# Performance work log

Hardware: AMD Instinct MI355X
Metric: run time of the kernel (lower is better)

The kernel has to match this reference:

```python
import jax, jax.numpy as jnp
import numpy as np

B, T, C, H, S = 4, 2048, 1024, 16, 64
LN_EPS = 1e-5
WKV_EPS = 1e-6
K_CLAMP = 30.0


def _ln(x, g, b):
    m = jnp.mean(x, axis=-1, keepdims=True)
    v = jnp.var(x, axis=-1, keepdims=True)
    return (x - m) * jax.lax.rsqrt(v + LN_EPS) * g + b


def _wkv(k, v, time_decay, time_first):
    # k, v: [B,T,H,S]; recurrence in fp32 over time
    decay = jnp.exp(-jnp.exp(time_decay.astype(jnp.float32)))  # [H,S]
    tf = jnp.exp(time_first.astype(jnp.float32))               # [H,S]
    kt = jnp.moveaxis(k, 1, 0).astype(jnp.float32)  # [T,B,H,S]
    vt = jnp.moveaxis(v, 1, 0).astype(jnp.float32)
    # t == 0 special case: state seeded with time_first factor
    w0 = jnp.exp(jnp.minimum(kt[0], K_CLAMP))
    num0 = tf * w0 * vt[0]
    den0 = tf * w0

    def step(carry, xs):
        num, den = carry
        kk, vv = xs
        w = jnp.exp(jnp.minimum(kk, K_CLAMP))
        num = decay * num + w * vv
        den = decay * den + w
        return (num, den), num / (den + WKV_EPS)

    (_, _), rest = jax.lax.scan(step, (num0, den0), (kt[1:], vt[1:]))
    out = jnp.concatenate([(num0 / (den0 + WKV_EPS))[None], rest], axis=0)  # [T,B,H,S]
    return jnp.moveaxis(out, 0, 1)  # [B,T,H,S]


def setup_inputs() -> dict:
    key = jax.random.key(0)
    ks = jax.random.split(key, 8)
    sc = 1.0 / np.sqrt(C)
    sc4 = 1.0 / np.sqrt(4 * C)
    return {
        "x": jax.random.normal(ks[0], (B, T, C), jnp.float32),
        "time_decay": jnp.full((H, S), -5.0, jnp.float32),
        "time_first": jnp.zeros((H, S), jnp.float32),
        "Wk": jax.random.normal(ks[1], (C, C), jnp.float32) * sc,
        "Wv": jax.random.normal(ks[2], (C, C), jnp.float32) * sc,
        "Wr": jax.random.normal(ks[3], (C, C), jnp.float32) * sc,
        "Wo": jax.random.normal(ks[4], (C, C), jnp.float32) * sc,
        "Wffk": jax.random.normal(ks[5], (4 * C, C), jnp.float32) * sc,
        "Wffv": jax.random.normal(ks[6], (C, 4 * C), jnp.float32) * sc4,
        "ln1_g": jnp.ones((C,), jnp.float32),
        "ln1_b": jnp.zeros((C,), jnp.float32),
        "ln2_g": jnp.ones((C,), jnp.float32),
        "ln2_b": jnp.zeros((C,), jnp.float32),
    }


def reference(x, time_decay, time_first, Wk, Wv, Wr, Wo, Wffk, Wffv, ln1_g, ln1_b, ln2_g, ln2_b):
    b, t, c = x.shape
    h, s = time_decay.shape
    xl = _ln(x, ln1_g, ln1_b)
    k = (xl @ Wk.T).reshape(b, t, h, s)
    v = (xl @ Wv.T).reshape(b, t, h, s)
    r = (xl @ Wr.T).reshape(b, t, h, s)
    wkv = _wkv(k, v, time_decay, time_first).astype(x.dtype)
    rwkv = (jax.nn.sigmoid(r) * wkv).reshape(b, t, c)
    x = x + rwkv @ Wo.T
    xl2 = _ln(x, ln2_g, ln2_b)
    ffn = (jax.nn.relu(xl2 @ Wffk.T) ** 2) @ Wffv.T
    return x + ffn
```

## Files before the change

### kernel.cpp

```cpp
#include <hip/hip_runtime.h>
#include <cstdint>
#include <cstddef>

#define TT 2048
#define CC 1024
#define HH 16
#define SS 64
#define MROWS 8192
#define KVRN 3072
#define NCH 32
#define LCH 64

using short8 = __attribute__((ext_vector_type(8))) short;
using f32x4  = __attribute__((ext_vector_type(4))) float;

__device__ __forceinline__ float b2f(unsigned short u) {
  union { unsigned int i; float f; } c; c.i = ((unsigned int)u) << 16; return c.f;
}
__device__ __forceinline__ unsigned short f2b(float f) {
  union { float f; unsigned int i; } c; c.f = f;
  unsigned int r = c.i + 0x7fffu + ((c.i >> 16) & 1u);
  return (unsigned short)(r >> 16);
}

typedef const __attribute__((address_space(1))) unsigned int* gas_ptr;
typedef __attribute__((address_space(3))) unsigned int* las_ptr;
__device__ __forceinline__ void gl_lds16(const unsigned short* g, unsigned short* l) {
  __builtin_amdgcn_global_load_lds((gas_ptr)g, (las_ptr)l, 16, 0, 0);
}

__global__ __launch_bounds__(256) void cvt_ln_kernel(const float* __restrict__ Wk,
                                                     const float* __restrict__ Wv,
                                                     const float* __restrict__ Wr,
                                                     const float* __restrict__ Wo,
                                                     const float* __restrict__ Wffk,
                                                     const float* __restrict__ Wffv,
                                                     unsigned short* __restrict__ dst,
                                                     const float* __restrict__ x,
                                                     const float* __restrict__ g,
                                                     const float* __restrict__ bta,
                                                     unsigned short* __restrict__ xlo,
                                                     float* __restrict__ x2o) {
  const size_t M1 = 1048576;
  const int tid = threadIdx.x;
  if (blockIdx.x < 12288) {
    size_t i = ((size_t)blockIdx.x * 256 + tid) * 4;
    const float* src; size_t off;
    if      (i <  1 * M1) { src = Wk;   off = 0;      }
    else if (i <  2 * M1) { src = Wv;   off = 1 * M1; }
    else if (i <  3 * M1) { src = Wr;   off = 2 * M1; }
    else if (i <  4 * M1) { src = Wo;   off = 3 * M1; }
    else if (i <  8 * M1) { src = Wffk; off = 4 * M1; }
    else                  { src = Wffv; off = 8 * M1; }
    float4 v = *(const float4*)(src + (i - off));
    *(ushort4*)(dst + i) = make_ushort4(f2b(v.x), f2b(v.y), f2b(v.z), f2b(v.w));
    return;
  }
  const int row = blockIdx.x - 12288;
  const float* xr = x + (size_t)row * CC;
  float4 v = *(const float4*)(xr + tid * 4);
  *(float4*)(x2o + (size_t)row * CC + tid * 4) = v;
  float s  = v.x + v.y + v.z + v.w;
  float ss = v.x * v.x + v.y * v.y + v.z * v.z + v.w * v.w;
#pragma unroll
  for (int off = 32; off > 0; off >>= 1) {
    s  += __shfl_xor(s, off, 64);
    ss += __shfl_xor(ss, off, 64);
  }
  __shared__ float ls[4], lss[4];
  if ((tid & 63) == 0) { ls[tid >> 6] = s; lss[tid >> 6] = ss; }
  __syncthreads();
  s  = ls[0] + ls[1] + ls[2] + ls[3];
  ss = lss[0] + lss[1] + lss[2] + lss[3];
  const float mean = s * (1.0f / CC);
  const float var  = ss * (1.0f / CC) - mean * mean;
  const float rstd = rsqrtf(var + 1e-5f);
  float4 gv = *(const float4*)(g + tid * 4);
  float4 bv = *(const float4*)(bta + tid * 4);
  ushort4 o = make_ushort4(f2b((v.x - mean) * rstd * gv.x + bv.x),
                           f2b((v.y - mean) * rstd * gv.y + bv.y),
                           f2b((v.z - mean) * rstd * gv.z + bv.z),
                           f2b((v.w - mean) * rstd * gv.w + bv.w));
  *(ushort4*)(xlo + (size_t)row * CC + tid * 4) = o;
}

__global__ __launch_bounds__(256) void ln_kernel(const float* __restrict__ x,
                                                 const float* __restrict__ g,
                                                 const float* __restrict__ bta,
                                                 unsigned short* __restrict__ out,
                                                 float* __restrict__ outc) {
  const int row = blockIdx.x;
  const int tid = threadIdx.x;
  const float* xr = x + (size_t)row * CC;
  float4 v = *(const float4*)(xr + tid * 4);
  *(float4*)(outc + (size_t)row * CC + tid * 4) = v;
  float s  = v.x + v.y + v.z + v.w;
  float ss = v.x * v.x + v.y * v.y + v.z * v.z + v.w * v.w;
#pragma unroll
  for (int off = 32; off > 0; off >>= 1) {
    s  += __shfl_xor(s, off, 64);
    ss += __shfl_xor(ss, off, 64);
  }
  __shared__ float ls[4], lss[4];
  if ((tid & 63) == 0) { ls[tid >> 6] = s; lss[tid >> 6] = ss; }
  __syncthreads();
  s  = ls[0] + ls[1] + ls[2] + ls[3];
  ss = lss[0] + lss[1] + lss[2] + lss[3];
  const float mean = s * (1.0f / CC);
  const float var  = ss * (1.0f / CC) - mean * mean;
  const float rstd = rsqrtf(var + 1e-5f);
  float4 gv = *(const float4*)(g + tid * 4);
  float4 bv = *(const float4*)(bta + tid * 4);
  ushort4 o = make_ushort4(f2b((v.x - mean) * rstd * gv.x + bv.x),
                           f2b((v.y - mean) * rstd * gv.y + bv.y),
                           f2b((v.z - mean) * rstd * gv.z + bv.z),
                           f2b((v.w - mean) * rstd * gv.w + bv.w));
  *(ushort4*)(out + (size_t)row * CC + tid * 4) = o;
}

__global__ __launch_bounds__(64) void wkv_local(const unsigned short* __restrict__ kvr,
                                                const float* __restrict__ td,
                                                const float* __restrict__ tfp,
                                                float* __restrict__ scratch) {
  const int blk = blockIdx.x;
  const int bh = blk >> 5, c = blk & (NCH - 1);
  const int b = bh >> 4, h = bh & 15;
  const int s = threadIdx.x;
  const int ch = h * SS + s;
  const float e = __expf(td[ch]);
  const float d = __expf(-e);
  const float tfir = __expf(tfp[ch]);
  size_t idx = ((size_t)b * TT + (size_t)c * LCH) * KVRN + ch;
  float num = 0.f, den = 0.f;
  for (int i = 0; i < LCH; ++i) {
    float w = __expf(fminf(b2f(kvr[idx]), 30.f));
    if (c == 0 && i == 0) w *= tfir;
    float vv = b2f(kvr[idx + 1024]);
    num = d * num + w * vv;
    den = d * den + w;
    idx += KVRN;
  }
  float* o = scratch + ((size_t)bh * NCH + c) * 128;
  o[s] = num; o[64 + s] = den;
}

__global__ __launch_bounds__(64) void wkv_emit(const unsigned short* __restrict__ kvr,
                                               const float* __restrict__ td,
                                               const float* __restrict__ tfp,
                                               const float* __restrict__ scratch,
                                               unsigned short* __restrict__ rwkv) {
  const int blk = blockIdx.x;
  const int bh = blk >> 5, c = blk & (NCH - 1);
  const int b = bh >> 4, h = bh & 15;
  const int s = threadIdx.x;
  const int ch = h * SS + s;
  const float e = __expf(td[ch]);
  const float d = __expf(-e);
  const float Dc = __expf(-e * (float)LCH);
  const float tfir = __expf(tfp[ch]);
  float num = 0.f, den = 0.f;
  const float* sc = scratch + (size_t)bh * NCH * 128;
  for (int cc = 0; cc < c; ++cc) {
    num = Dc * num + sc[cc * 128 + s];
    den = Dc * den + sc[cc * 128 + 64 + s];
  }
  size_t idx = ((size_t)b * TT + (size_t)c * LCH) * KVRN + ch;
  size_t odx = ((size_t)b * TT + (size_t)c * LCH) * CC + ch;
  for (int i = 0; i < LCH; ++i) {
    float w = __expf(fminf(b2f(kvr[idx]), 30.f));
    if (c == 0 && i == 0) w *= tfir;
    float vv = b2f(kvr[idx + 1024]);
    num = d * num + w * vv;
    den = d * den + w;
    float o = num / (den + 1e-6f);
    float rr = b2f(kvr[idx + 2048]);
    float sg = 1.0f / (1.0f + __expf(-rr));
    rwkv[odx] = f2b(sg * o);
    idx += KVRN;
    odx += CC;
  }
}

template <int EP>
__global__ __launch_bounds__(256, 3) void gemm_bt(const unsigned short* __restrict__ A,
                                                  const unsigned short* __restrict__ Bw,
                                                  void* __restrict__ outv,
                                                  const float* __restrict__ res,
                                                  int N, int K) {
  __shared__ __align__(16) unsigned short As[3][128 * 32];
  __shared__ __align__(16) unsigned short Bs[3][128 * 32];
  const int tid = threadIdx.x;

  const int nbn = N >> 7;
  const int per_grp = nbn << 4;
  const int bid = blockIdx.x;
  const int grp = bid / per_grp;
  const int rem = bid - grp * per_grp;
  const int bm = (grp << 4) + (rem & 15);
  const int bn = rem >> 4;

  const int ch0 = tid, ch1 = tid + 256;
  const int r0 = ch0 >> 2, q0 = (ch0 & 3) ^ ((ch0 >> 3) & 3);
  const int r1 = ch1 >> 2, q1 = (ch1 & 3) ^ ((ch1 >> 3) & 3);
  const unsigned short* ga0 = A  + (size_t)(bm * 128 + r0) * K + q0 * 8;
  const unsigned short* ga1 = A  + (size_t)(bm * 128 + r1) * K + q1 * 8;
  const unsigned short* gb0 = Bw + (size_t)(bn * 128 + r0) * K + q0 * 8;
  const unsigned short* gb1 = Bw + (size_t)(bn * 128 + r1) * K + q1 * 8;
  const int so0 = ch0 * 8, so1 = ch1 * 8;

  const int lane = tid & 63;
  const int w    = tid >> 6;
  const int q    = lane >> 4, r16 = lane & 15;
  const int qs   = q ^ ((r16 >> 1) & 3);
  const int wrow = (w >> 1) * 64, wcol = (w & 1) * 64;

  f32x4 acc[4][4] = {};

  auto stage = [&](int b3) {
    gl_lds16(ga0, &As[b3][so0]);
    gl_lds16(ga1, &As[b3][so1]);
    gl_lds16(gb0, &Bs[b3][so0]);
    gl_lds16(gb1, &Bs[b3][so1]);
    ga0 += 32; ga1 += 32; gb0 += 32; gb1 += 32;
  };

  const int iters = K >> 5;
  stage(0);
  stage(1);

  int cb = 0, pb = 2;
  for (int i = 0; i < iters; ++i) {
    __builtin_amdgcn_s_waitcnt(0x0F74);
    __builtin_amdgcn_sched_barrier(0);
    asm volatile("s_barrier");
    __builtin_amdgcn_sched_barrier(0);
    if (i + 2 < iters) stage(pb);

    const unsigned short* Ab = &As[cb][0];
    const unsigned short* Bb = &Bs[cb][0];
    short8 af[4], bfr[4];
#pragma unroll
    for (int mi = 0; mi < 4; ++mi)
      af[mi] = *(const short8*)(Ab + ((wrow + mi * 16 + r16) * 4 + qs) * 8);
#pragma unroll
    for (int ni = 0; ni < 4; ++ni)
      bfr[ni] = *(const short8*)(Bb + ((wcol + ni * 16 + r16) * 4 + qs) * 8);
#pragma unroll
    for (int mi = 0; mi < 4; ++mi)
#pragma unroll
      for (int ni = 0; ni < 4; ++ni)
        acc[mi][ni] = __builtin_amdgcn_mfma_f32_16x16x32_bf16(af[mi], bfr[ni], acc[mi][ni], 0, 0, 0);

    cb = (cb == 2) ? 0 : cb + 1;
    pb = (pb == 2) ? 0 : pb + 1;
  }

#pragma unroll
  for (int mi = 0; mi < 4; ++mi) {
#pragma unroll
    for (int r = 0; r < 4; ++r) {
      const int grow = bm * 128 + wrow + mi * 16 + q * 4 + r;
#pragma unroll
      for (int ni = 0; ni < 4; ++ni) {
        const int gcol = bn * 128 + wcol + ni * 16 + r16;
        const size_t idx = (size_t)grow * N + gcol;
        float vv = acc[mi][ni][r];
        if (EP == 2) {
          ((float*)outv)[idx] = res[idx] + vv;
        } else {
          if (EP == 1) { vv = fmaxf(vv, 0.0f); vv = vv * vv; }
          ((unsigned short*)outv)[idx] = f2b(vv);
        }
      }
    }
  }
}

template <int EP>
__global__ __launch_bounds__(256, 2) void gemm_wide(const unsigned short* __restrict__ A,
                                                    const unsigned short* __restrict__ Bw,
                                                    void* __restrict__ outv,
                                                    int N, int Kfull, int Kloop) {
  __shared__ __align__(16) unsigned short As[3][256 * 32];
  __shared__ __align__(16) unsigned short Bs[3][128 * 32];
  const int tid = threadIdx.x;

  const int nbn = N >> 7;
  const int per_grp = nbn << 4;
  const int bid = blockIdx.x;
  const int grp = bid / per_grp;
  const int rem = bid - grp * per_grp;
  const int bm = (grp << 4) + (rem & 15);
  const int bn = rem >> 4;
  const int koffb = blockIdx.y * Kloop;
  const int iters = Kloop >> 5;

  const int r0  = tid >> 2;
  const int qsl = ((tid & 3) ^ ((tid >> 3) & 3)) << 3;
  const unsigned short* gA[4];
  const unsigned short* gB[2];
#pragma unroll
  for (int m = 0; m < 4; ++m)
    gA[m] = A + (size_t)(bm * 256 + r0 + 64 * m) * Kfull + koffb + qsl;
#pragma unroll
  for (int m = 0; m < 2; ++m)
    gB[m] = Bw + (size_t)(bn * 128 + r0 + 64 * m) * Kfull + koffb + qsl;
  const int so = tid * 8;

  auto stage = [&](int b3) {
    unsigned short* da = &As[b3][0];
    unsigned short* db = &Bs[b3][0];
#pragma unroll
    for (int m = 0; m < 4; ++m) { gl_lds16(gA[m], da + so + 2048 * m); gA[m] += 32; }
#pragma unroll
    for (int m = 0; m < 2; ++m) { gl_lds16(gB[m], db + so + 2048 * m); gB[m] += 32; }
  };

  const int lane = tid & 63;
  const int w    = tid >> 6;
  const int q    = lane >> 4, r16 = lane & 15;
  const int qs   = q ^ ((r16 >> 1) & 3);
  const int wrow = (w >> 1) * 128, wcol = (w & 1) * 64;

  f32x4 acc[8][4] = {};

  stage(0);
  stage(1);

  int cb = 0, pb = 2;
  for (int i = 0; i < iters; ++i) {
    __builtin_amdgcn_s_waitcnt(0x0F76);
    __builtin_amdgcn_sched_barrier(0);
    asm volatile("s_barrier");
    __builtin_amdgcn_sched_barrier(0);
    if (i + 2 < iters) stage(pb);

    const unsigned short* Ab = &As[cb][0];
    const unsigned short* Bb = &Bs[cb][0];
    short8 af[8], bfr[4];
#pragma unroll
    for (int mi = 0; mi < 8; ++mi)
      af[mi] = *(const short8*)(Ab + ((wrow + mi * 16 + r16) * 4 + qs) * 8);
#pragma unroll
    for (int ni = 0; ni < 4; ++ni)
      bfr[ni] = *(const short8*)(Bb + ((wcol + ni * 16 + r16) * 4 + qs) * 8);
#pragma unroll
    for (int mi = 0; mi < 8; ++mi)
#pragma unroll
      for (int ni = 0; ni < 4; ++ni)
        acc[mi][ni] = __builtin_amdgcn_mfma_f32_16x16x32_bf16(af[mi], bfr[ni], acc[mi][ni], 0, 0, 0);

    cb = (cb == 2) ? 0 : cb + 1;
    pb = (pb == 2) ? 0 : pb + 1;
  }

#pragma unroll
  for (int mi = 0; mi < 8; ++mi) {
#pragma unroll
    for (int r = 0; r < 4; ++r) {
      const int grow = bm * 256 + wrow + mi * 16 + q * 4 + r;
#pragma unroll
      for (int ni = 0; ni < 4; ++ni) {
        const int gcol = bn * 128 + wcol + ni * 16 + r16;
        const size_t idx = (size_t)grow * N + gcol;
        float vv = acc[mi][ni][r];
        if (EP == 3) {
          unsafeAtomicAdd((float*)outv + idx, vv);
        } else {
          if (EP == 1) { vv = fmaxf(vv, 0.0f); vv = vv * vv; }
          ((unsigned short*)outv)[idx] = f2b(vv);
        }
      }
    }
  }
}

extern "C" void kernel_launch(void* const* d_in, const int* in_sizes, int n_in,
                              void* d_out, int out_size, void* d_ws, size_t ws_size,
                              hipStream_t stream) {
  const float* x    = (const float*)d_in[0];
  const float* td   = (const float*)d_in[1];
  const float* tf   = (const float*)d_in[2];
  const float* Wk   = (const float*)d_in[3];
  const float* Wv   = (const float*)d_in[4];
  const float* Wr   = (const float*)d_in[5];
  const float* Wo   = (const float*)d_in[6];
  const float* Wffk = (const float*)d_in[7];
  const float* Wffv = (const float*)d_in[8];
  const float* g1   = (const float*)d_in[9];
  const float* b1   = (const float*)d_in[10];
  const float* g2   = (const float*)d_in[11];
  const float* b2   = (const float*)d_in[12];
  float* out = (float*)d_out;

  char* ws = (char*)d_ws;
  const size_t MB = 1024ull * 1024ull;
  unsigned short* WB    = (unsigned short*)ws;
  unsigned short* WkvrB = WB;
  unsigned short* WoB   = WB + 3 * 1048576;
  unsigned short* WfkB  = WB + 4 * 1048576;
  unsigned short* WfvB  = WB + 8 * 1048576;
  unsigned short* xl    = (unsigned short*)(ws + 24 * MB);
  unsigned short* kvr   = (unsigned short*)(ws + 40 * MB);
  float*          x2    = (float*)(ws + 88 * MB);
  unsigned short* hb    = (unsigned short*)(ws + 120 * MB);
  float*          wkvS  = (float*)(ws + 184 * MB);
  unsigned short* rwkv  = xl;
  unsigned short* xl2   = kvr;

  cvt_ln_kernel<<<12288 + MROWS, 256, 0, stream>>>(Wk, Wv, Wr, Wo, Wffk, Wffv, WB,
                                                   x, g1, b1, xl, x2);

  gemm_bt<0><<<(KVRN / 128) * (MROWS / 128), 256, 0, stream>>>(xl, WkvrB, kvr, nullptr, KVRN, 1024);

  wkv_local<<<64 * NCH, 64, 0, stream>>>(kvr, td, tf, wkvS);
  wkv_emit<<<64 * NCH, 64, 0, stream>>>(kvr, td, tf, wkvS, rwkv);

  gemm_wide<3><<<dim3((MROWS / 256) * (CC / 128), 2), 256, 0, stream>>>(
      rwkv, WoB, x2, CC, 1024, 512);

  ln_kernel<<<MROWS, 256, 0, stream>>>(x2, g2, b2, xl2, out);

  gemm_wide<1><<<dim3((MROWS / 256) * (4096 / 128), 1), 256, 0, stream>>>(
      xl2, WfkB, hb, 4096, 1024, 1024);

  gemm_wide<3><<<dim3((MROWS / 256) * (CC / 128), 2), 256, 0, stream>>>(
      hb, WfvB, out, CC, 4096, 2048);
}
```

Before: 503.4 us.

## Use 512-thread GEMM for FFN and fused-residual gemm_bt for Wo projection

The wide GEMM now runs 8 waves of 512 threads instead of 4, each wave computing a 64x64 sub-tile, so fewer accumulator registers are needed per wave and occupancy can rise. The output projection switches from a split-K atomic-add GEMM into a pre-copied x2 buffer to gemm_bt with its residual epilogue, which writes x + result directly. This removes the x copy from the LayerNorm kernel and the atomics. The tradeoff is lower per-wave reuse in the FFN GEMMs and no split-K parallelism for Wo.

```diff
diff --git a/kernel.cpp b/kernel.cpp
--- a/kernel.cpp
+++ b/kernel.cpp
@@ -39,8 +39,7 @@
                                                      const float* __restrict__ x,
                                                      const float* __restrict__ g,
                                                      const float* __restrict__ bta,
-                                                     unsigned short* __restrict__ xlo,
-                                                     float* __restrict__ x2o) {
+                                                     unsigned short* __restrict__ xlo) {
   const size_t M1 = 1048576;
   const int tid = threadIdx.x;
   if (blockIdx.x < 12288) {
@@ -59,7 +58,6 @@
   const int row = blockIdx.x - 12288;
   const float* xr = x + (size_t)row * CC;
   float4 v = *(const float4*)(xr + tid * 4);
-  *(float4*)(x2o + (size_t)row * CC + tid * 4) = v;
   float s  = v.x + v.y + v.z + v.w;
   float ss = v.x * v.x + v.y * v.y + v.z * v.z + v.w * v.w;
 #pragma unroll
@@ -277,10 +275,10 @@
 }
 
 template <int EP>
-__global__ __launch_bounds__(256, 2) void gemm_wide(const unsigned short* __restrict__ A,
-                                                    const unsigned short* __restrict__ Bw,
-                                                    void* __restrict__ outv,
-                                                    int N, int Kfull, int Kloop) {
+__global__ __launch_bounds__(512, 2) void gemm512(const unsigned short* __restrict__ A,
+                                                  const unsigned short* __restrict__ Bw,
+                                                  void* __restrict__ outv,
+                                                  int N, int Kfull, int Kloop) {
   __shared__ __align__(16) unsigned short As[3][256 * 32];
   __shared__ __align__(16) unsigned short Bs[3][128 * 32];
   const int tid = threadIdx.x;
@@ -297,39 +295,34 @@
 
   const int r0  = tid >> 2;
   const int qsl = ((tid & 3) ^ ((tid >> 3) & 3)) << 3;
-  const unsigned short* gA[4];
-  const unsigned short* gB[2];
-#pragma unroll
-  for (int m = 0; m < 4; ++m)
-    gA[m] = A + (size_t)(bm * 256 + r0 + 64 * m) * Kfull + koffb + qsl;
-#pragma unroll
-  for (int m = 0; m < 2; ++m)
-    gB[m] = Bw + (size_t)(bn * 128 + r0 + 64 * m) * Kfull + koffb + qsl;
+  const unsigned short* gA0 = A  + (size_t)(bm * 256 + r0) * Kfull + koffb + qsl;
+  const unsigned short* gA1 = gA0 + (size_t)128 * Kfull;
+  const unsigned short* gB0 = Bw + (size_t)(bn * 128 + r0) * Kfull + koffb + qsl;
   const int so = tid * 8;
 
   auto stage = [&](int b3) {
     unsigned short* da = &As[b3][0];
     unsigned short* db = &Bs[b3][0];
-#pragma unroll
-    for (int m = 0; m < 4; ++m) { gl_lds16(gA[m], da + so + 2048 * m); gA[m] += 32; }
-#pragma unroll
-    for (int m = 0; m < 2; ++m) { gl_lds16(gB[m], db + so + 2048 * m); gB[m] += 32; }
+    gl_lds16(gA0, da + so);
+    gl_lds16(gA1, da + so + 4096);
+    gl_lds16(gB0, db + so);
+    gA0 += 32; gA1 += 32; gB0 += 32;
   };
 
   const int lane = tid & 63;
   const int w    = tid >> 6;
   const int q    = lane >> 4, r16 = lane & 15;
   const int qs   = q ^ ((r16 >> 1) & 3);
-  const int wrow = (w >> 1) * 128, wcol = (w & 1) * 64;
-
-  f32x4 acc[8][4] = {};
+  const int wrow = (w >> 1) * 64, wcol = (w & 1) * 64;
+
+  f32x4 acc[4][4] = {};
 
   stage(0);
   stage(1);
 
   int cb = 0, pb = 2;
   for (int i = 0; i < iters; ++i) {
-    __builtin_amdgcn_s_waitcnt(0x0F76);
+    __builtin_amdgcn_s_waitcnt(0x0F73);
     __builtin_amdgcn_sched_barrier(0);
     asm volatile("s_barrier");
     __builtin_amdgcn_sched_barrier(0);
@@ -337,15 +330,15 @@
 
     const unsigned short* Ab = &As[cb][0];
     const unsigned short* Bb = &Bs[cb][0];
-    short8 af[8], bfr[4];
-#pragma unroll
-    for (int mi = 0; mi < 8; ++mi)
+    short8 af[4], bfr[4];
+#pragma unroll
+    for (int mi = 0; mi < 4; ++mi)
       af[mi] = *(const short8*)(Ab + ((wrow + mi * 16 + r16) * 4 + qs) * 8);
 #pragma unroll
     for (int ni = 0; ni < 4; ++ni)
       bfr[ni] = *(const short8*)(Bb + ((wcol + ni * 16 + r16) * 4 + qs) * 8);
 #pragma unroll
-    for (int mi = 0; mi < 8; ++mi)
+    for (int mi = 0; mi < 4; ++mi)
 #pragma unroll
       for (int ni = 0; ni < 4; ++ni)
         acc[mi][ni] = __builtin_amdgcn_mfma_f32_16x16x32_bf16(af[mi], bfr[ni], acc[mi][ni], 0, 0, 0);
@@ -355,7 +348,7 @@
   }
 
 #pragma unroll
-  for (int mi = 0; mi < 8; ++mi) {
+  for (int mi = 0; mi < 4; ++mi) {
 #pragma unroll
     for (int r = 0; r < 4; ++r) {
       const int grow = bm * 256 + wrow + mi * 16 + q * 4 + r;
@@ -409,21 +402,20 @@
   unsigned short* xl2   = kvr;
 
   cvt_ln_kernel<<<12288 + MROWS, 256, 0, stream>>>(Wk, Wv, Wr, Wo, Wffk, Wffv, WB,
-                                                   x, g1, b1, xl, x2);
+                                                   x, g1, b1, xl);
 
   gemm_bt<0><<<(KVRN / 128) * (MROWS / 128), 256, 0, stream>>>(xl, WkvrB, kvr, nullptr, KVRN, 1024);
 
   wkv_local<<<64 * NCH, 64, 0, stream>>>(kvr, td, tf, wkvS);
   wkv_emit<<<64 * NCH, 64, 0, stream>>>(kvr, td, tf, wkvS, rwkv);
 
-  gemm_wide<3><<<dim3((MROWS / 256) * (CC / 128), 2), 256, 0, stream>>>(
-      rwkv, WoB, x2, CC, 1024, 512);
+  gemm_bt<2><<<(CC / 128) * (MROWS / 128), 256, 0, stream>>>(rwkv, WoB, x2, x, 1024, 1024);
 
   ln_kernel<<<MROWS, 256, 0, stream>>>(x2, g2, b2, xl2, out);
 
-  gemm_wide<1><<<dim3((MROWS / 256) * (4096 / 128), 1), 256, 0, stream>>>(
+  gemm512<1><<<dim3((MROWS / 256) * (4096 / 128), 1), 512, 0, stream>>>(
       xl2, WfkB, hb, 4096, 1024, 1024);
 
-  gemm_wide<3><<<dim3((MROWS / 256) * (CC / 128), 2), 256, 0, stream>>>(
+  gemm512<3><<<dim3((MROWS / 256) * (CC / 128), 2), 512, 0, stream>>>(
       hb, WfvB, out, CC, 4096, 2048);
 }
```

Measured after the change: 457.1 us. 9.2% less time.
